# Kernel tuning notes

Hardware: AMD Instinct MI355X
Metric: run time of the kernel (lower is better)

## Reference

```python
import jax, jax.numpy as jnp
import numpy as np

EMSIZE = 2048
NCLASS = 128
D1 = 2
D2 = 2
NSENT = 32768


def setup_inputs() -> dict:
    key = jax.random.key(0)
    k1, k2, k3 = jax.random.split(key, 3)
    x = jax.random.normal(k1, (NSENT, 1, EMSIZE), dtype=jnp.float32)
    # Scaled-normal params (original uses nn.init.normal_; scaling keeps tanh unsaturated)
    W1 = jax.random.normal(k2, (D1 + 1, EMSIZE, NCLASS), dtype=jnp.float32) / np.float32(np.sqrt(EMSIZE))
    b1 = jnp.zeros((1, NCLASS), dtype=jnp.float32)
    W2 = jax.random.normal(k3, (D2 + 1, NCLASS, NCLASS), dtype=jnp.float32) / np.float32(np.sqrt(NCLASS))
    b2 = jnp.zeros((1, NCLASS), dtype=jnp.float32)
    return {"structural_representations": x, "W1": W1, "b1": b1, "W2": W2, "b2": b2}


def _shift_down(y, k, n):
    # y[p] -> y[p-k], zeros for p < k (causal shift along sentence axis)
    return jnp.pad(y, ((k, 0), (0, 0)))[:n] if k > 0 else y


def reference(structural_representations, W1, b1, W2, b2):
    x = structural_representations  # [N, 1, E]
    n, _, e = x.shape
    d1 = W1.shape[0] - 1
    d2 = W2.shape[0] - 1
    c = W1.shape[-1]
    xs = x.reshape(n, e)  # [N, E]

    # Stage 1: S[p] = sum_{k=0..d1, k<=p} (x[p-k] @ W1[k] + b1)
    Y = jnp.einsum('ne,kec->knc', xs, W1)  # [d1+1, N, C]: one big GEMM per tap
    S = sum(_shift_down(Y[k], k, n) for k in range(d1 + 1))  # windowed causal sum
    pos = jnp.arange(n)
    cnt1 = (jnp.minimum(pos, d1) + 1).astype(xs.dtype)  # bias added once per valid tap
    H = jnp.tanh(S + cnt1[:, None] * b1[0])  # [N, C]

    # Stage 2 (i >= d2): Z[i] = sum_{j=0..d2} H[i-d2+j] @ W2[j] + (d2+1)*b2
    G = jnp.einsum('nc,kcd->knd', H, W2)  # [d2+1, N, C]
    Z = sum(_shift_down(G[j], d2 - j, n) for j in range(d2 + 1)) + (d2 + 1) * b2[0]

    # Fallback for i < d2: single term tanh(x[i]@W1[0]+b1) @ W2[0] + b2
    H0 = jnp.tanh(xs @ W1[0] + b1[0])
    Z0 = H0 @ W2[0] + b2[0]
    Z = jnp.where((pos >= d2)[:, None], Z, Z0)

    out = jax.nn.log_softmax(Z, axis=-1)
    return out.reshape(n, 1, c)
```

## Files before the change

kernel.cpp:

```cpp
#include <hip/hip_runtime.h>
#include <math.h>

typedef __attribute__((ext_vector_type(8))) short short8;
typedef __attribute__((ext_vector_type(4))) float f32x4;

#define MFMA16(a, b, c) __builtin_amdgcn_mfma_f32_16x16x32_bf16((a), (b), (c), 0, 0, 0)

__device__ inline void gl_lds16(const void* g, void* l) {
  __builtin_amdgcn_global_load_lds(
      (const __attribute__((address_space(1))) void*)g,
      (__attribute__((address_space(3))) void*)l, 16, 0, 0);
}

__device__ inline unsigned int pack2(float lo, float hi) {
  unsigned int ulo = __float_as_uint(lo), uhi = __float_as_uint(hi);
  return (uhi & 0xFFFF0000u) | (ulo >> 16);
}
__device__ inline unsigned short f2bf_r(float f) {
  return (unsigned short)((__float_as_uint(f) + 0x8000u) >> 16);
}
__device__ inline float bf2f(unsigned short h) {
  return __uint_as_float(((unsigned int)h) << 16);
}

__global__ __launch_bounds__(256) void k_repack(const float* __restrict__ W1,
                                                const float* __restrict__ W2,
                                                unsigned short* __restrict__ W1bt,
                                                unsigned short* __restrict__ W2t) {
  __shared__ float tile[64 * 128];
  const int b = blockIdx.x, tid = threadIdx.x;
  if (b < 96) {
    const int k = b >> 5, et = b & 31;
    const int e0 = et * 64;
    const float* src = W1 + (size_t)k * 262144 + (size_t)e0 * 128;
#pragma unroll
    for (int i = 0; i < 8; ++i) {
      int idx4 = tid + i * 256;
      ((f32x4*)tile)[idx4] = ((const f32x4*)src)[idx4];
    }
    __syncthreads();
#pragma unroll
    for (int i = 0; i < 4; ++i) {
      int item = tid + i * 256;
      int c = item >> 3, eo = (item & 7) * 8;
      union { unsigned short h[8]; uint4 v; } t;
#pragma unroll
      for (int u = 0; u < 8; ++u) t.h[u] = f2bf_r(tile[(eo + u) * 128 + c]);
      *(uint4*)(W1bt + (size_t)(k * 128 + c) * 2048 + e0 + eo) = t.v;
    }
  } else {
    int idx = (b - 96) * 256 + tid;
    int j = idx >> 14, r = idx & 16383, d = r >> 7, c = r & 127;
    W2t[idx] = f2bf_r(W2[(size_t)j * 16384 + (size_t)c * 128 + d]);
  }
}

__global__ __launch_bounds__(512, 4) void k_fused(const float* __restrict__ X,
                                                  const unsigned short* __restrict__ Bt,
                                                  const unsigned short* __restrict__ W2t,
                                                  const float* __restrict__ b1,
                                                  const float* __restrict__ b2,
                                                  float* __restrict__ out) {
  __shared__ __align__(16) char smem[66560];
  float* Alds = (float*)smem;
  unsigned short* Blds = (unsigned short*)(smem + 17408);
  unsigned short* Yt = (unsigned short*)smem;
  float* zbuf = (float*)(smem + 62720);

  const int r0 = blockIdx.x * 64;
  const int tid = threadIdx.x, wave = tid >> 6, lane = tid & 63;
  const int mrow = lane & 15, quad = lane >> 4;

  const float* agp[3];
#pragma unroll
  for (int r = 0; r < 2; ++r) {
    int i = wave * 8 + r * 4 + (lane >> 4);
    int g = r0 - 4 + i; if (g < 0) g = 0;
    int c = (lane & 15) ^ (i & 15);
    agp[r] = X + (size_t)g * 2048 + c * 4;
  }
  {
    int i = 64 + (lane >> 4);
    int g = r0 - 4 + i; if (g > 32767) g = 32767;
    int c = (lane & 15) ^ (i & 15);
    agp[2] = X + (size_t)g * 2048 + c * 4;
  }
  const unsigned short* bgp[6];
#pragma unroll
  for (int r = 0; r < 6; ++r) {
    int col = (wave * 6 + r) * 8 + (lane >> 3);
    int c = (lane & 7) ^ (col & 7);
    bgp[r] = Bt + (size_t)col * 2048 + c * 8;
  }

  f32x4 acc[5][3] = {};

  for (int k0 = 0; k0 < 2048; k0 += 64) {
#pragma unroll
    for (int r = 0; r < 2; ++r)
      gl_lds16(agp[r], (char*)Alds + (wave * 8 + r * 4) * 256);
    if (wave == 0) gl_lds16(agp[2], (char*)Alds + 64 * 256);
#pragma unroll
    for (int r = 0; r < 6; ++r)
      gl_lds16(bgp[r], (char*)Blds + (wave * 6 + r) * 1024);
#pragma unroll
    for (int r = 0; r < 3; ++r) agp[r] += 64;
#pragma unroll
    for (int r = 0; r < 6; ++r) bgp[r] += 64;
    __syncthreads();

#pragma unroll
    for (int s = 0; s < 2; ++s) {
      short8 af[5];
#pragma unroll
      for (int rt = 0; rt < 5; ++rt) {
        int row = rt * 16 + mrow;
        int c0 = s * 8 + quad * 2;
        const float* base = Alds + row * 64;
        f32x4 x0 = *(const f32x4*)(base + ((c0 ^ mrow) * 4));
        f32x4 x1 = *(const f32x4*)(base + (((c0 + 1) ^ mrow) * 4));
        union { unsigned int u[4]; short8 v; } t;
        t.u[0] = pack2(x0[0], x0[1]); t.u[1] = pack2(x0[2], x0[3]);
        t.u[2] = pack2(x1[0], x1[1]); t.u[3] = pack2(x1[2], x1[3]);
        af[rt] = t.v;
      }
#pragma unroll
      for (int ct = 0; ct < 3; ++ct) {
        int col = wave * 48 + ct * 16 + mrow;
        int ch = (s * 4 + quad) ^ (mrow & 7);
        short8 bf = *(const short8*)(Blds + col * 64 + ch * 8);
#pragma unroll
        for (int rt = 0; rt < 5; ++rt)
          acc[rt][ct] = MFMA16(af[rt], bf, acc[rt][ct]);
      }
    }
    __syncthreads();
  }

#pragma unroll
  for (int rt = 0; rt < 5; ++rt)
#pragma unroll
    for (int ct = 0; ct < 3; ++ct)
#pragma unroll
      for (int rg = 0; rg < 4; ++rg) {
        int l = rt * 16 + quad * 4 + rg;
        int col = wave * 48 + ct * 16 + mrow;
        Yt[l * 392 + col] = f2bf_r(acc[rt][ct][rg]);
      }
  __syncthreads();

  for (int idx = tid; idx < 66 * 128; idx += 512) {
    int hl = idx >> 7, c = idx & 127;
    int p = r0 - 2 + hl;
    int i = hl + 2;
    float h = 0.f;
    if (p >= 0) {
      float s = bf2f(Yt[i * 392 + c]);
      float cnt = 1.f;
      if (p >= 1) { s += bf2f(Yt[(i - 1) * 392 + 128 + c]); cnt += 1.f; }
      if (p >= 2) { s += bf2f(Yt[(i - 2) * 392 + 256 + c]); cnt += 1.f; }
      h = tanhf(fmaf(cnt, b1[c], s));
    }
    Yt[(i - 2) * 392 + 256 + c] = f2bf_r(h);
  }
  __syncthreads();

  if (wave < 4) {
    f32x4 acc2[8] = {};
#pragma unroll
    for (int j = 0; j < 3; ++j) {
#pragma unroll
      for (int kk = 0; kk < 4; ++kk) {
        short8 a0 = *(const short8*)&Yt[(wave * 16 + mrow + j) * 392 + 256 + kk * 32 + quad * 8];
        const unsigned short* wp = W2t + (size_t)(j * 128 + mrow) * 128 + kk * 32 + quad * 8;
#pragma unroll
        for (int ct = 0; ct < 8; ++ct)
          acc2[ct] = MFMA16(a0, *(const short8*)(wp + ct * 16 * 128), acc2[ct]);
      }
    }

#pragma unroll
    for (int rg = 0; rg < 4; ++rg) {
      float z[8]; float m = -1e30f;
#pragma unroll
      for (int ct = 0; ct < 8; ++ct) {
        z[ct] = acc2[ct][rg] + 3.f * b2[ct * 16 + mrow];
        m = fmaxf(m, z[ct]);
      }
#pragma unroll
      for (int off = 1; off < 16; off <<= 1) m = fmaxf(m, __shfl_xor(m, off, 64));
      float s = 0.f;
#pragma unroll
      for (int ct = 0; ct < 8; ++ct) s += __expf(z[ct] - m);
#pragma unroll
      for (int off = 1; off < 16; off <<= 1) s += __shfl_xor(s, off, 64);
      float lse = m + __logf(s);
      int grow = r0 + wave * 16 + quad * 4 + rg;
      if (grow >= 2) {
        float* op = out + (size_t)grow * 128 + mrow;
#pragma unroll
        for (int ct = 0; ct < 8; ++ct) op[ct * 16] = z[ct] - lse;
      }
    }
  }

  if (blockIdx.x == 0) {
    __syncthreads();
    int row = tid >> 7, d = tid & 127;
    if (tid < 256)
      zbuf[row * 128 + d] = tanhf(bf2f(Yt[(row + 4) * 392 + d]) + b1[d]);
    __syncthreads();
    float zv = 0.f;
    if (tid < 256) {
      zv = b2[d];
      for (int c = 0; c < 128; ++c)
        zv = fmaf(zbuf[row * 128 + c], bf2f(W2t[(size_t)d * 128 + c]), zv);
    }
    __syncthreads();
    if (tid < 256) zbuf[row * 128 + d] = zv;
    __syncthreads();
    if (tid < 256) {
      float m = -1e30f;
      for (int c = 0; c < 128; ++c) m = fmaxf(m, zbuf[row * 128 + c]);
      float s = 0.f;
      for (int c = 0; c < 128; ++c) s += __expf(zbuf[row * 128 + c] - m);
      out[(size_t)row * 128 + d] = zv - m - __logf(s);
    }
  }
}

extern "C" void kernel_launch(void* const* d_in, const int* in_sizes, int n_in,
                              void* d_out, int out_size, void* d_ws, size_t ws_size,
                              hipStream_t stream) {
  const float* X  = (const float*)d_in[0];
  const float* W1 = (const float*)d_in[1];
  const float* b1 = (const float*)d_in[2];
  const float* W2 = (const float*)d_in[3];
  const float* b2 = (const float*)d_in[4];
  float* out = (float*)d_out;

  unsigned short* W1bt = (unsigned short*)d_ws;
  unsigned short* W2t  = (unsigned short*)((char*)d_ws + 1572864);

  k_repack<<<288, 256, 0, stream>>>(W1, W2, W1bt, W2t);
  k_fused<<<512, 512, 0, stream>>>(X, W1bt, W2t, b1, b2, out);
}
```

Baseline: 421.9 us.

## Double-buffer bf16 A tiles in LDS and stream B fragments from global

The main GEMM loop is reorganised. Each thread prefetches its slice of X into registers and converts it to bf16 once, then writes it into one of two LDS buffers, so the next tile fills while the current one is computed and each iteration needs a single barrier. B fragments are read straight from global memory into registers in MFMA operand layout, bypassing LDS. This removes the fp32 A staging and the per-wave repeated conversion, and halves LDS use for A. The cost is more register pressure and exposed global latency on the B loads.

```diff
diff --git a/kernel.cpp b/kernel.cpp
--- a/kernel.cpp
+++ b/kernel.cpp
@@ -5,12 +5,6 @@
 typedef __attribute__((ext_vector_type(4))) float f32x4;
 
 #define MFMA16(a, b, c) __builtin_amdgcn_mfma_f32_16x16x32_bf16((a), (b), (c), 0, 0, 0)
-
-__device__ inline void gl_lds16(const void* g, void* l) {
-  __builtin_amdgcn_global_load_lds(
-      (const __attribute__((address_space(1))) void*)g,
-      (__attribute__((address_space(3))) void*)l, 16, 0, 0);
-}
 
 __device__ inline unsigned int pack2(float lo, float hi) {
   unsigned int ulo = __float_as_uint(lo), uhi = __float_as_uint(hi);
@@ -61,9 +55,7 @@
                                                   const float* __restrict__ b1,
                                                   const float* __restrict__ b2,
                                                   float* __restrict__ out) {
-  __shared__ __align__(16) char smem[66560];
-  float* Alds = (float*)smem;
-  unsigned short* Blds = (unsigned short*)(smem + 17408);
+  __shared__ __align__(16) char smem[63744];
   unsigned short* Yt = (unsigned short*)smem;
   float* zbuf = (float*)(smem + 62720);
 
@@ -71,71 +63,93 @@
   const int tid = threadIdx.x, wave = tid >> 6, lane = tid & 63;
   const int mrow = lane & 15, quad = lane >> 4;
 
-  const float* agp[3];
-#pragma unroll
-  for (int r = 0; r < 2; ++r) {
-    int i = wave * 8 + r * 4 + (lane >> 4);
-    int g = r0 - 4 + i; if (g < 0) g = 0;
-    int c = (lane & 15) ^ (i & 15);
-    agp[r] = X + (size_t)g * 2048 + c * 4;
-  }
+  const float *ap0, *ap1, *ap2;
+  int lw0, lw1, lw2;
   {
-    int i = 64 + (lane >> 4);
-    int g = r0 - 4 + i; if (g > 32767) g = 32767;
-    int c = (lane & 15) ^ (i & 15);
-    agp[2] = X + (size_t)g * 2048 + c * 4;
-  }
-  const unsigned short* bgp[6];
-#pragma unroll
-  for (int r = 0; r < 6; ++r) {
-    int col = (wave * 6 + r) * 8 + (lane >> 3);
-    int c = (lane & 7) ^ (col & 7);
-    bgp[r] = Bt + (size_t)col * 2048 + c * 8;
-  }
+    int u, r_, o_, g;
+    u = tid;           r_ = u >> 4; o_ = u & 15;
+    g = r0 - 4 + r_; if (g < 0) g = 0;
+    ap0 = X + (size_t)g * 2048 + o_ * 4;
+    lw0 = r_ * 128 + (((o_ >> 1) ^ (r_ & 7)) << 4) + ((o_ & 1) << 3);
+    u = tid + 512;     r_ = u >> 4; o_ = u & 15;
+    g = r0 - 4 + r_; if (g < 0) g = 0;
+    ap1 = X + (size_t)g * 2048 + o_ * 4;
+    lw1 = r_ * 128 + (((o_ >> 1) ^ (r_ & 7)) << 4) + ((o_ & 1) << 3);
+    u = 1024 + (tid - 448); if (u < 1024) u = 1024;
+    r_ = u >> 4; o_ = u & 15;
+    g = r0 - 4 + r_;
+    ap2 = X + (size_t)g * 2048 + o_ * 4;
+    lw2 = r_ * 128 + (((o_ >> 1) ^ (r_ & 7)) << 4) + ((o_ & 1) << 3);
+  }
+  f32x4 ar0, ar1, ar2;
+
+  const unsigned short* bp0 = Bt + (size_t)(wave * 48 +  0 + mrow) * 2048 + quad * 8;
+  const unsigned short* bp1 = Bt + (size_t)(wave * 48 + 16 + mrow) * 2048 + quad * 8;
+  const unsigned short* bp2 = Bt + (size_t)(wave * 48 + 32 + mrow) * 2048 + quad * 8;
+  short8 bfr[3][2];
 
   f32x4 acc[5][3] = {};
 
-  for (int k0 = 0; k0 < 2048; k0 += 64) {
-#pragma unroll
-    for (int r = 0; r < 2; ++r)
-      gl_lds16(agp[r], (char*)Alds + (wave * 8 + r * 4) * 256);
-    if (wave == 0) gl_lds16(agp[2], (char*)Alds + 64 * 256);
-#pragma unroll
-    for (int r = 0; r < 6; ++r)
-      gl_lds16(bgp[r], (char*)Blds + (wave * 6 + r) * 1024);
-#pragma unroll
-    for (int r = 0; r < 3; ++r) agp[r] += 64;
-#pragma unroll
-    for (int r = 0; r < 6; ++r) bgp[r] += 64;
-    __syncthreads();
-
+  auto loadA = [&]() {
+    ar0 = *(const f32x4*)ap0; ap0 += 64;
+    ar1 = *(const f32x4*)ap1; ap1 += 64;
+    if (wave == 7) { ar2 = *(const f32x4*)ap2; ap2 += 64; }
+  };
+  auto convA = [&](char* buf) {
+    uint2 v;
+    v.x = pack2(ar0[0], ar0[1]); v.y = pack2(ar0[2], ar0[3]);
+    *(uint2*)(buf + lw0) = v;
+    v.x = pack2(ar1[0], ar1[1]); v.y = pack2(ar1[2], ar1[3]);
+    *(uint2*)(buf + lw1) = v;
+    if (wave == 7) {
+      v.x = pack2(ar2[0], ar2[1]); v.y = pack2(ar2[2], ar2[3]);
+      *(uint2*)(buf + lw2) = v;
+    }
+  };
+  auto loadB = [&]() {
+    bfr[0][0] = *(const short8*)(bp0); bfr[0][1] = *(const short8*)(bp0 + 32);
+    bfr[1][0] = *(const short8*)(bp1); bfr[1][1] = *(const short8*)(bp1 + 32);
+    bfr[2][0] = *(const short8*)(bp2); bfr[2][1] = *(const short8*)(bp2 + 32);
+    bp0 += 64; bp1 += 64; bp2 += 64;
+  };
+  auto compute = [&](const char* buf) {
 #pragma unroll
     for (int s = 0; s < 2; ++s) {
+      const int swz = (((s * 4 + quad) ^ (mrow & 7)) << 4);
       short8 af[5];
 #pragma unroll
+      for (int rt = 0; rt < 5; ++rt)
+        af[rt] = *(const short8*)(buf + (rt * 16 + mrow) * 128 + swz);
+#pragma unroll
       for (int rt = 0; rt < 5; ++rt) {
-        int row = rt * 16 + mrow;
-        int c0 = s * 8 + quad * 2;
-        const float* base = Alds + row * 64;
-        f32x4 x0 = *(const f32x4*)(base + ((c0 ^ mrow) * 4));
-        f32x4 x1 = *(const f32x4*)(base + (((c0 + 1) ^ mrow) * 4));
-        union { unsigned int u[4]; short8 v; } t;
-        t.u[0] = pack2(x0[0], x0[1]); t.u[1] = pack2(x0[2], x0[3]);
-        t.u[2] = pack2(x1[0], x1[1]); t.u[3] = pack2(x1[2], x1[3]);
-        af[rt] = t.v;
-      }
-#pragma unroll
-      for (int ct = 0; ct < 3; ++ct) {
-        int col = wave * 48 + ct * 16 + mrow;
-        int ch = (s * 4 + quad) ^ (mrow & 7);
-        short8 bf = *(const short8*)(Blds + col * 64 + ch * 8);
-#pragma unroll
-        for (int rt = 0; rt < 5; ++rt)
-          acc[rt][ct] = MFMA16(af[rt], bf, acc[rt][ct]);
-      }
-    }
-    __syncthreads();
-  }
+        acc[rt][0] = MFMA16(af[rt], bfr[0][s], acc[rt][0]);
+        acc[rt][1] = MFMA16(af[rt], bfr[1][s], acc[rt][1]);
+        acc[rt][2] = MFMA16(af[rt], bfr[2][s], acc[rt][2]);
+      }
+    }
+  };
+
+  loadA();
+  convA(smem);
+  loadB();
+  loadA();
+  asm volatile("s_waitcnt lgkmcnt(0)" ::: "memory");
+  __builtin_amdgcn_s_barrier();
+  __builtin_amdgcn_sched_barrier(0);
+
+#pragma unroll 2
+  for (int t = 0; t < 32; ++t) {
+    compute(smem + (t & 1) * 8704);
+    if (t < 31) {
+      convA(smem + ((t + 1) & 1) * 8704);
+      loadB();
+      if (t < 30) loadA();
+      asm volatile("s_waitcnt lgkmcnt(0)" ::: "memory");
+      __builtin_amdgcn_s_barrier();
+      __builtin_amdgcn_sched_barrier(0);
+    }
+  }
+  __syncthreads();
 
 #pragma unroll
   for (int rt = 0; rt < 5; ++rt)
```

Result: slower. 492.1 us (+16.6%).
